# Performance work log

Hardware: AMD Instinct MI355X
Metric: run time of the kernel (lower is better)

The kernel has to match this reference:

```python
import jax, jax.numpy as jnp
import numpy as np

N = 10000
E = 160000
B = 16
NEG_SLOPE = 0.2


def gat_conv(x, src, dst, W, a_src, a_dst, b, heads, ch):
    # x: [N, F_in]; src/dst: [E'] (self-loops included); W: [F_in, heads*ch]
    n = x.shape[0]
    h = (x @ W).reshape(n, heads, ch)                     # [N,H,C]
    alpha_src = jnp.sum(h * a_src, axis=-1)               # [N,H]
    alpha_dst = jnp.sum(h * a_dst, axis=-1)               # [N,H]
    e = jax.nn.leaky_relu(alpha_src[src] + alpha_dst[dst], NEG_SLOPE)  # [E,H]
    # segment softmax over edges grouped by destination node
    m = jax.ops.segment_max(e, dst, num_segments=n)       # [N,H]
    ex = jnp.exp(e - m[dst])                              # [E,H]
    denom = jax.ops.segment_sum(ex, dst, num_segments=n)  # [N,H]
    alpha = ex / denom[dst]                               # [E,H]
    out = jax.ops.segment_sum(alpha[:, :, None] * h[src], dst, num_segments=n)  # [N,H,C]
    return out.reshape(n, heads * ch) + b


def setup_inputs() -> dict:
    key = jax.random.key(0)
    ks = jax.random.split(key, 16)
    glorot = lambda k, shp: jax.random.normal(k, shp, jnp.float32) * np.sqrt(2.0 / (shp[0] + shp[-1]))
    inp = {
        "x": jax.random.normal(ks[0], (N, 128), jnp.float32),
        "edge_index": jax.random.randint(ks[1], (2, E), 0, N, jnp.int64),
        "batch": jnp.sort(jax.random.randint(ks[2], (N,), 0, B, jnp.int64)),
        # conv1: 128 -> 128 per head, 8 heads
        "W1": glorot(ks[3], (128, 8 * 128)),
        "att_src1": glorot(ks[4], (8, 128)),
        "att_dst1": glorot(ks[5], (8, 128)),
        "b1": jnp.zeros((8 * 128,), jnp.float32),
        # conv2: 1024 -> 64 per head, 8 heads
        "W2": glorot(ks[6], (1024, 8 * 64)),
        "att_src2": glorot(ks[7], (8, 64)),
        "att_dst2": glorot(ks[8], (8, 64)),
        "b2": jnp.zeros((8 * 64,), jnp.float32),
        "fc1_w": glorot(ks[9], (512, 32)),
        "fc1_b": jnp.zeros((32,), jnp.float32),
        "fc2_w": glorot(ks[10], (32, 10)),
        "fc2_b": jnp.zeros((10,), jnp.float32),
    }
    return inp


def reference(x, edge_index, batch, W1, att_src1, att_dst1, b1,
              W2, att_src2, att_dst2, b2, fc1_w, fc1_b, fc2_w, fc2_b):
    n = x.shape[0]
    loop = jnp.arange(n, dtype=edge_index.dtype)
    src = jnp.concatenate([edge_index[0], loop])  # PyG add_self_loops=True
    dst = jnp.concatenate([edge_index[1], loop])
    h = jax.nn.elu(gat_conv(x, src, dst, W1, att_src1, att_dst1, b1, 8, 128))   # [N,1024]
    h = jax.nn.elu(gat_conv(h, src, dst, W2, att_src2, att_dst2, b2, 8, 64))    # [N,512]
    # global mean pool over graphs
    sums = jax.ops.segment_sum(h, batch, num_segments=B)                        # [B,512]
    cnt = jax.ops.segment_sum(jnp.ones((n,), h.dtype), batch, num_segments=B)
    g = sums / jnp.maximum(cnt, 1.0)[:, None]
    g = jax.nn.elu(g @ fc1_w + fc1_b)
    return g @ fc2_w + fc2_b                                                    # [B,10]
```

## Files before the change

### kernel.cpp

```cpp
#include <hip/hip_runtime.h>
#include <math.h>

#define HEADS 8
#define NEG 0.2f

typedef unsigned short ushort_t;
typedef __attribute__((ext_vector_type(8))) short short8;
typedef float f32x4 __attribute__((ext_vector_type(4)));

__device__ inline ushort_t f2bf(float f) {
  union { float f; unsigned u; } v; v.f = f;
  unsigned r = (v.u + 0x7FFF + ((v.u >> 16) & 1)) >> 16;
  return (ushort_t)r;
}

__device__ inline float4 bf4(uint2 v) {
  union { unsigned u; float f; } a, b, c, d;
  a.u = v.x << 16; b.u = v.x & 0xffff0000u;
  c.u = v.y << 16; d.u = v.y & 0xffff0000u;
  return make_float4(a.f, b.f, c.f, d.f);
}

__device__ inline float elu_f(float v) {
  return (v > 0.f) ? v : (__expf(v) - 1.f);
}

__global__ void zero_k(int* __restrict__ p, int n) {
  int i = blockIdx.x * blockDim.x + threadIdx.x;
  int stride = gridDim.x * blockDim.x;
  for (; i < n; i += stride) p[i] = 0;
}

__global__ void prep_k(const int* __restrict__ ei, int* __restrict__ src,
                       int* __restrict__ dst, int* __restrict__ deg, int E, int Nn) {
  int i = blockIdx.x * blockDim.x + threadIdx.x;
  if (i >= E + Nn) return;
  int s, d;
  if (i < E) { s = ei[i]; d = ei[E + i]; }
  else       { s = d = i - E; }
  src[i] = s;
  dst[i] = d;
  atomicAdd(&deg[d], 1);
}

__global__ __launch_bounds__(1024) void scan_k(const int* __restrict__ deg,
                                               int* __restrict__ offs,
                                               int* __restrict__ cursor, int Nn) {
  __shared__ int wtot[16];
  __shared__ int wexcl[16];
  __shared__ int soff_s;
  int t = threadIdx.x;
  int lane = t & 63, w = t >> 6;
  if (t == 0) soff_s = 0;
  __syncthreads();
  for (int base = 0; base < Nn; base += 4096) {
    int idx = base + 4 * t;
    int4 v = make_int4(0, 0, 0, 0);
    if (idx + 3 < Nn) v = *(const int4*)&deg[idx];
    else {
      if (idx < Nn)     v.x = deg[idx];
      if (idx + 1 < Nn) v.y = deg[idx + 1];
      if (idx + 2 < Nn) v.z = deg[idx + 2];
      if (idx + 3 < Nn) v.w = deg[idx + 3];
    }
    int s1 = v.x, s2 = s1 + v.y, s3 = s2 + v.z, s4 = s3 + v.w;
    int sc = s4;
#pragma unroll
    for (int o = 1; o < 64; o <<= 1) {
      int x = __shfl_up(sc, o);
      if (lane >= o) sc += x;
    }
    if (lane == 63) wtot[w] = sc;
    __syncthreads();
    if (w == 0) {
      int tv = (lane < 16) ? wtot[lane] : 0;
      int ts = tv;
#pragma unroll
      for (int o = 1; o < 16; o <<= 1) {
        int x = __shfl_up(ts, o);
        if (lane >= o) ts += x;
      }
      if (lane < 16) wexcl[lane] = ts - tv;
      if (lane == 15) wtot[15] = ts;
    }
    __syncthreads();
    int excl = soff_s + wexcl[w] + (sc - s4);
    int o0 = excl, o1 = excl + s1, o2 = excl + s2, o3 = excl + s3;
    if (idx < Nn)     { offs[idx] = o0;     cursor[idx] = o0; }
    if (idx + 1 < Nn) { offs[idx + 1] = o1; cursor[idx + 1] = o1; }
    if (idx + 2 < Nn) { offs[idx + 2] = o2; cursor[idx + 2] = o2; }
    if (idx + 3 < Nn) { offs[idx + 3] = o3; cursor[idx + 3] = o3; }
    int chunk_total = wtot[15];
    __syncthreads();
    if (t == 0) soff_s += chunk_total;
    __syncthreads();
  }
  if (t == 0) offs[Nn] = soff_s;
}

__global__ void scatter_k(const int* __restrict__ src, const int* __restrict__ dst,
                          int* __restrict__ cursor, int* __restrict__ psrc, int Etot) {
  int i = blockIdx.x * blockDim.x + threadIdx.x;
  if (i >= Etot) return;
  int p = atomicAdd(&cursor[dst[i]], 1);
  psrc[p] = src[i];
}

__global__ void cast_k(const float* __restrict__ in, ushort_t* __restrict__ out, int n4) {
  int i = blockIdx.x * blockDim.x + threadIdx.x;
  if (i >= n4) return;
  float4 v = ((const float4*)in)[i];
  ushort_t o[4] = {f2bf(v.x), f2bf(v.y), f2bf(v.z), f2bf(v.w)};
  *(uint2*)&out[i * 4] = *(uint2*)o;
}

__global__ void tcast_k(const float* __restrict__ W, ushort_t* __restrict__ Wt, int K, int N) {
  int idx = blockIdx.x * blockDim.x + threadIdx.x;
  if (idx >= K * N) return;
  int n = idx / K, k = idx - n * K;
  Wt[idx] = f2bf(W[(size_t)k * N + n]);
}

#define LDA 40
__global__ __launch_bounds__(256) void mfma_gemm_k(const ushort_t* __restrict__ A,
                                                   const ushort_t* __restrict__ Bt,
                                                   ushort_t* __restrict__ Cb,
                                                   const float* __restrict__ att_s,
                                                   const float* __restrict__ att_d,
                                                   float* __restrict__ asrc,
                                                   float* __restrict__ adst,
                                                   int M, int N, int K, int CSHIFT) {
  __shared__ ushort_t As[128 * LDA];
  __shared__ ushort_t Bs[128 * LDA];
  int tid = threadIdx.x;
  int lane = tid & 63;
  int wave = tid >> 6;
  int wm = (wave >> 1) * 64, wn = (wave & 1) * 64;
  int bm = blockIdx.y * 128, bn = blockIdx.x * 128;
  int lrow = lane & 15, lq = lane >> 4;

  f32x4 acc[4][4];
#pragma unroll
  for (int i = 0; i < 4; i++)
#pragma unroll
    for (int j = 0; j < 4; j++) acc[i][j] = 0.f;

  int srow = tid >> 2;
  int skc = (tid & 3) * 8;

  int gr0 = min(bm + srow, M - 1);
  int gr1 = min(bm + srow + 64, M - 1);
  const ushort_t* pa0 = &A[(size_t)gr0 * K + skc];
  const ushort_t* pa1 = &A[(size_t)gr1 * K + skc];
  const ushort_t* pb0 = &Bt[(size_t)(bn + srow) * K + skc];
  const ushort_t* pb1 = &Bt[(size_t)(bn + srow + 64) * K + skc];

  short8 va0 = *(const short8*)pa0;
  short8 va1 = *(const short8*)pa1;
  short8 vb0 = *(const short8*)pb0;
  short8 vb1 = *(const short8*)pb1;

  for (int k0 = 0; k0 < K; k0 += 32) {
    __syncthreads();
    *(short8*)&As[srow * LDA + skc] = va0;
    *(short8*)&As[(srow + 64) * LDA + skc] = va1;
    *(short8*)&Bs[srow * LDA + skc] = vb0;
    *(short8*)&Bs[(srow + 64) * LDA + skc] = vb1;
    __syncthreads();
    if (k0 + 32 < K) {
      va0 = *(const short8*)(pa0 + k0 + 32);
      va1 = *(const short8*)(pa1 + k0 + 32);
      vb0 = *(const short8*)(pb0 + k0 + 32);
      vb1 = *(const short8*)(pb1 + k0 + 32);
    }
    short8 af[4], bfr[4];
#pragma unroll
    for (int t = 0; t < 4; t++) {
      af[t]  = *(const short8*)&As[(wm + t * 16 + lrow) * LDA + lq * 8];
      bfr[t] = *(const short8*)&Bs[(wn + t * 16 + lrow) * LDA + lq * 8];
    }
#pragma unroll
    for (int i = 0; i < 4; i++)
#pragma unroll
      for (int j = 0; j < 4; j++)
        acc[i][j] = __builtin_amdgcn_mfma_f32_16x16x32_bf16(af[i], bfr[j], acc[i][j], 0, 0, 0);
  }

  {
    int hh = (bn + wn) >> CSHIFT;
    float avs[4], avd[4];
#pragma unroll
    for (int j = 0; j < 4; j++) {
      int col = bn + wn + j * 16 + lrow;
      avs[j] = att_s[col];
      avd[j] = att_d[col];
    }
#pragma unroll
    for (int i = 0; i < 4; i++) {
#pragma unroll
      for (int r = 0; r < 4; r++) {
        float ps = 0.f, pd = 0.f;
#pragma unroll
        for (int j = 0; j < 4; j++) {
          float v = acc[i][j][r];
          ps += v * avs[j];
          pd += v * avd[j];
        }
#pragma unroll
        for (int o = 1; o < 16; o <<= 1) {
          ps += __shfl_xor(ps, o);
          pd += __shfl_xor(pd, o);
        }
        int row = bm + wm + i * 16 + lq * 4 + r;
        if (lrow == 0 && row < M) {
          atomicAdd(&asrc[row * HEADS + hh], ps);
          atomicAdd(&adst[row * HEADS + hh], pd);
        }
      }
    }
  }

#pragma unroll
  for (int i = 0; i < 4; i++) {
    int row0 = bm + wm + i * 16 + lq * 4;
#pragma unroll
    for (int j = 0; j < 4; j++) {
      int col = bn + wn + j * 16 + lrow;
#pragma unroll
      for (int r = 0; r < 4; r++) {
        int row = row0 + r;
        if (row < M) Cb[(size_t)row * N + col] = f2bf(acc[i][j][r]);
      }
    }
  }
}

template <int F, int CSHIFT, int BT, int NSPLIT, typename OT>
__global__ __launch_bounds__(BT) void aggregate_k(const ushort_t* __restrict__ hb,
                                                  const float* __restrict__ asrc,
                                                  const float* __restrict__ adst,
                                                  const int* __restrict__ offs,
                                                  const int* __restrict__ psrc,
                                                  const float* __restrict__ bias,
                                                  OT* __restrict__ out) {
  constexpr int CPB = F / NSPLIT;
  static_assert(CPB == 4 * BT, "CPB/thread mismatch");
  int nb = blockIdx.x;
  int n = nb / NSPLIT;
  int coff = (nb - n * NSPLIT) * CPB;
  int t = threadIdx.x;
  int c0 = coff + 4 * t;
  int hh = c0 >> CSHIFT;
  float adn = adst[n * HEADS + hh];
  int e0 = offs[n], e1 = offs[n + 1];
  float4 acc = make_float4(0.f, 0.f, 0.f, 0.f);
  float wsum = 0.f;

  int i = e0;
  int s[8];
  if (i + 8 <= e1) {
#pragma unroll
    for (int u = 0; u < 8; u++) s[u] = psrc[i + u];
  }
  while (i + 8 <= e1) {
    uint2 r[8];
    float av[8];
#pragma unroll
    for (int u = 0; u < 8; u++) r[u] = *(const uint2*)&hb[(size_t)s[u] * F + c0];
#pragma unroll
    for (int u = 0; u < 8; u++) av[u] = asrc[s[u] * HEADS + hh];
    i += 8;
    bool more = (i + 8 <= e1);
    int sn[8];
#pragma unroll
    for (int u = 0; u < 8; u++) sn[u] = more ? psrc[i + u] : 0;
#pragma unroll
    for (int u = 0; u < 8; u++) {
      float v = av[u] + adn;
      v = (v > 0.f) ? v : NEG * v;
      float w = __expf(v);
      float4 f = bf4(r[u]);
      wsum += w;
      acc.x += w * f.x;
      acc.y += w * f.y;
      acc.z += w * f.z;
      acc.w += w * f.w;
    }
#pragma unroll
    for (int u = 0; u < 8; u++) s[u] = sn[u];
  }
  for (; i < e1; i++) {
    int ss = psrc[i];
    float v = asrc[ss * HEADS + hh] + adn;
    v = (v > 0.f) ? v : NEG * v;
    float w = __expf(v);
    float4 f = bf4(*(const uint2*)&hb[(size_t)ss * F + c0]);
    wsum += w;
    acc.x += w * f.x; acc.y += w * f.y;
    acc.z += w * f.z; acc.w += w * f.w;
  }

  float inv = 1.f / wsum;
  float v0 = elu_f(acc.x * inv + bias[c0]);
  float v1 = elu_f(acc.y * inv + bias[c0 + 1]);
  float v2 = elu_f(acc.z * inv + bias[c0 + 2]);
  float v3 = elu_f(acc.w * inv + bias[c0 + 3]);
  if (sizeof(OT) == 2) {
    unsigned p0 = (unsigned)f2bf(v0) | ((unsigned)f2bf(v1) << 16);
    unsigned p1 = (unsigned)f2bf(v2) | ((unsigned)f2bf(v3) << 16);
    *(uint2*)&((ushort_t*)out)[(size_t)n * F + c0] = make_uint2(p0, p1);
  } else {
    *(float4*)&((float*)out)[(size_t)n * F + c0] = make_float4(v0, v1, v2, v3);
  }
}

__global__ void bounds_k(const int* __restrict__ batch, int* __restrict__ bstart,
                         int* __restrict__ bend, int Nn) {
  int i = blockIdx.x * blockDim.x + threadIdx.x;
  if (i >= Nn) return;
  int b = batch[i];
  if (i == 0 || batch[i - 1] != b) bstart[b] = i;
  if (i == Nn - 1 || batch[i + 1] != b) bend[b] = i + 1;
}

__global__ __launch_bounds__(256) void pool_k(const float* __restrict__ g,
                                              const int* __restrict__ batch,
                                              float* __restrict__ sums, int Nn) {
  int c = blockIdx.x * 256 + threadIdx.x;
  int n0 = blockIdx.y * 50;
  int n1 = min(n0 + 50, Nn);
  if (n0 >= n1) return;
  float acc = 0.f;
  int cur = batch[n0];
  for (int n = n0; n < n1; n++) {
    int b = batch[n];
    if (b != cur) { atomicAdd(&sums[cur * 512 + c], acc); acc = 0.f; cur = b; }
    acc += g[(size_t)n * 512 + c];
  }
  atomicAdd(&sums[cur * 512 + c], acc);
}

__global__ __launch_bounds__(512) void mlp_k(const float* __restrict__ sums,
                                             const int* __restrict__ bstart,
                                             const int* __restrict__ bend,
                                             const float* __restrict__ w1,
                                             const float* __restrict__ b1,
                                             const float* __restrict__ w2,
                                             const float* __restrict__ b2,
                                             float* __restrict__ out) {
  __shared__ float gm[16 * 512];
  __shared__ float t1[16 * 32];
  int t = threadIdx.x;
  for (int i = t; i < 16 * 512; i += 512) {
    int b = i >> 9;
    float c = (float)(bend[b] - bstart[b]);
    gm[i] = sums[i] / fmaxf(c, 1.f);
  }
  __syncthreads();
  {
    int b = t >> 5, j = t & 31;
    float s = b1[j];
    for (int k = 0; k < 512; k++) s += gm[(b << 9) + k] * w1[k * 32 + j];
    t1[t] = elu_f(s);
  }
  __syncthreads();
  if (t < 160) {
    int b = t / 10, j = t - b * 10;
    float s = b2[j];
#pragma unroll
    for (int k = 0; k < 32; k++) s += t1[b * 32 + k] * w2[k * 10 + j];
    out[t] = s;
  }
}

extern "C" void kernel_launch(void* const* d_in, const int* in_sizes, int n_in,
                              void* d_out, int out_size, void* d_ws, size_t ws_size,
                              hipStream_t stream) {
  const float* x   = (const float*)d_in[0];
  const int*   ei  = (const int*)d_in[1];
  const int* batch = (const int*)d_in[2];
  const float* W1  = (const float*)d_in[3];
  const float* as1 = (const float*)d_in[4];
  const float* ad1 = (const float*)d_in[5];
  const float* b1  = (const float*)d_in[6];
  const float* W2  = (const float*)d_in[7];
  const float* as2 = (const float*)d_in[8];
  const float* ad2 = (const float*)d_in[9];
  const float* b2  = (const float*)d_in[10];
  const float* f1w = (const float*)d_in[11];
  const float* f1b = (const float*)d_in[12];
  const float* f2w = (const float*)d_in[13];
  const float* f2b = (const float*)d_in[14];
  float* out = (float*)d_out;

  const int Nn = in_sizes[2];
  const int E = in_sizes[1] / 2;
  const int Etot = E + Nn;

  size_t off = 0;
  auto alloc = [&](size_t elems) { size_t o = off; off += (elems + 63) & ~(size_t)63; return o; };
  int* wsi = (int*)d_ws;
  float* wsf = (float*)d_ws;

  size_t o_deg  = alloc(Nn);
  size_t o_pool = alloc(16 * 512);
  size_t o_bst  = alloc(64);
  size_t o_ben  = alloc(64);
  size_t o_as1  = alloc((size_t)Nn * 8);
  size_t o_ad1  = alloc((size_t)Nn * 8);
  size_t o_as2  = alloc((size_t)Nn * 8);
  size_t o_ad2  = alloc((size_t)Nn * 8);
  size_t zero_words = off;
  size_t o_offs = alloc(Nn + 1);
  size_t o_cur  = alloc(Nn);
  size_t o_src  = alloc(Etot);
  size_t o_dst  = alloc(Etot);
  size_t o_psrc = alloc(Etot);
  size_t o_xb   = alloc((size_t)Nn * 128 / 2);
  size_t o_w1t  = alloc(1024 * 128 / 2);
  size_t o_w2t  = alloc(512 * 1024 / 2);
  size_t o_h    = alloc((size_t)Nn * 1024 / 2);
  size_t o_g    = alloc((size_t)Nn * 1024);

  ushort_t* xb  = (ushort_t*)(wsi + o_xb);
  ushort_t* w1t = (ushort_t*)(wsi + o_w1t);
  ushort_t* w2t = (ushort_t*)(wsi + o_w2t);
  ushort_t* hb  = (ushort_t*)(wsi + o_h);
  ushort_t* g1b = (ushort_t*)(wsi + o_g);

  int eb = (Etot + 255) / 256;

  zero_k<<<512, 256, 0, stream>>>(wsi, (int)zero_words);
  prep_k<<<eb, 256, 0, stream>>>(ei, wsi + o_src, wsi + o_dst, wsi + o_deg, E, Nn);
  scan_k<<<1, 1024, 0, stream>>>(wsi + o_deg, wsi + o_offs, wsi + o_cur, Nn);
  scatter_k<<<eb, 256, 0, stream>>>(wsi + o_src, wsi + o_dst, wsi + o_cur,
                                    wsi + o_psrc, Etot);

  cast_k<<<(Nn * 128 / 4 + 255) / 256, 256, 0, stream>>>(x, xb, Nn * 128 / 4);
  tcast_k<<<(128 * 1024 + 255) / 256, 256, 0, stream>>>(W1, w1t, 128, 1024);
  tcast_k<<<(1024 * 512 + 255) / 256, 256, 0, stream>>>(W2, w2t, 1024, 512);

  mfma_gemm_k<<<dim3(1024 / 128, (Nn + 127) / 128), 256, 0, stream>>>(
      xb, w1t, hb, as1, ad1, wsf + o_as1, wsf + o_ad1, Nn, 1024, 128, 7);
  aggregate_k<1024, 7, 128, 2, ushort_t><<<Nn * 2, 128, 0, stream>>>(
      hb, wsf + o_as1, wsf + o_ad1, wsi + o_offs, wsi + o_psrc, b1, g1b);

  mfma_gemm_k<<<dim3(512 / 128, (Nn + 127) / 128), 256, 0, stream>>>(
      g1b, w2t, hb, as2, ad2, wsf + o_as2, wsf + o_ad2, Nn, 512, 1024, 6);
  aggregate_k<512, 6, 64, 2, float><<<Nn * 2, 64, 0, stream>>>(
      hb, wsf + o_as2, wsf + o_ad2, wsi + o_offs, wsi + o_psrc, b2, wsf + o_g);

  bounds_k<<<(Nn + 255) / 256, 256, 0, stream>>>(batch, wsi + o_bst, wsi + o_ben, Nn);
  pool_k<<<dim3(2, (Nn + 49) / 50), 256, 0, stream>>>(wsf + o_g, batch, wsf + o_pool, Nn);
  mlp_k<<<1, 512, 0, stream>>>(wsf + o_pool, wsi + o_bst, wsi + o_ben, f1w, f1b, f2w, f2b, out);
}
```

Baseline: 284.8 us.

## Fuse cast/bounds launches into existing kernels and double GEMM K-tile to 64

Result: faster. 277.8 us (-2.5%).

```diff
diff --git a/kernel.cpp b/kernel.cpp
--- a/kernel.cpp
+++ b/kernel.cpp
@@ -32,8 +32,15 @@
 }
 
 __global__ void prep_k(const int* __restrict__ ei, int* __restrict__ src,
-                       int* __restrict__ dst, int* __restrict__ deg, int E, int Nn) {
+                       int* __restrict__ dst, int* __restrict__ deg,
+                       const int* __restrict__ batch, int* __restrict__ bstart,
+                       int* __restrict__ bend, int E, int Nn) {
   int i = blockIdx.x * blockDim.x + threadIdx.x;
+  if (i < Nn) {
+    int b = batch[i];
+    if (i == 0 || batch[i - 1] != b) bstart[b] = i;
+    if (i == Nn - 1 || batch[i + 1] != b) bend[b] = i + 1;
+  }
   if (i >= E + Nn) return;
   int s, d;
   if (i < E) { s = ei[i]; d = ei[E + i]; }
@@ -106,22 +113,27 @@
   psrc[p] = src[i];
 }
 
-__global__ void cast_k(const float* __restrict__ in, ushort_t* __restrict__ out, int n4) {
+__global__ void castall_k(const float* __restrict__ x, ushort_t* __restrict__ xb,
+                          const float* __restrict__ W1, ushort_t* __restrict__ w1t,
+                          const float* __restrict__ W2, ushort_t* __restrict__ w2t,
+                          int nx4) {
   int i = blockIdx.x * blockDim.x + threadIdx.x;
-  if (i >= n4) return;
-  float4 v = ((const float4*)in)[i];
-  ushort_t o[4] = {f2bf(v.x), f2bf(v.y), f2bf(v.z), f2bf(v.w)};
-  *(uint2*)&out[i * 4] = *(uint2*)o;
-}
-
-__global__ void tcast_k(const float* __restrict__ W, ushort_t* __restrict__ Wt, int K, int N) {
-  int idx = blockIdx.x * blockDim.x + threadIdx.x;
-  if (idx >= K * N) return;
-  int n = idx / K, k = idx - n * K;
-  Wt[idx] = f2bf(W[(size_t)k * N + n]);
-}
-
-#define LDA 40
+  if (i < nx4) {
+    float4 v = ((const float4*)x)[i];
+    ushort_t o[4] = {f2bf(v.x), f2bf(v.y), f2bf(v.z), f2bf(v.w)};
+    *(uint2*)&xb[i * 4] = *(uint2*)o;
+  }
+  if (i < 128 * 1024) {
+    int n = i >> 7, k = i & 127;
+    w1t[i] = f2bf(W1[(size_t)k * 1024 + n]);
+  }
+  if (i < 1024 * 512) {
+    int n = i >> 10, k = i & 1023;
+    w2t[i] = f2bf(W2[(size_t)k * 512 + n]);
+  }
+}
+
+#define LDA 72
 __global__ __launch_bounds__(256) void mfma_gemm_k(const ushort_t* __restrict__ A,
                                                    const ushort_t* __restrict__ Bt,
                                                    ushort_t* __restrict__ Cb,
@@ -156,34 +168,50 @@
   const ushort_t* pb1 = &Bt[(size_t)(bn + srow + 64) * K + skc];
 
   short8 va0 = *(const short8*)pa0;
-  short8 va1 = *(const short8*)pa1;
+  short8 va1 = *(const short8*)(pa0 + 32);
+  short8 va2 = *(const short8*)pa1;
+  short8 va3 = *(const short8*)(pa1 + 32);
   short8 vb0 = *(const short8*)pb0;
-  short8 vb1 = *(const short8*)pb1;
-
-  for (int k0 = 0; k0 < K; k0 += 32) {
+  short8 vb1 = *(const short8*)(pb0 + 32);
+  short8 vb2 = *(const short8*)pb1;
+  short8 vb3 = *(const short8*)(pb1 + 32);
+
+  for (int k0 = 0; k0 < K; k0 += 64) {
     __syncthreads();
     *(short8*)&As[srow * LDA + skc] = va0;
-    *(short8*)&As[(srow + 64) * LDA + skc] = va1;
+    *(short8*)&As[srow * LDA + 32 + skc] = va1;
+    *(short8*)&As[(srow + 64) * LDA + skc] = va2;
+    *(short8*)&As[(srow + 64) * LDA + 32 + skc] = va3;
     *(short8*)&Bs[srow * LDA + skc] = vb0;
-    *(short8*)&Bs[(srow + 64) * LDA + skc] = vb1;
-    __syncthreads();
-    if (k0 + 32 < K) {
-      va0 = *(const short8*)(pa0 + k0 + 32);
-      va1 = *(const short8*)(pa1 + k0 + 32);
-      vb0 = *(const short8*)(pb0 + k0 + 32);
-      vb1 = *(const short8*)(pb1 + k0 + 32);
-    }
-    short8 af[4], bfr[4];
-#pragma unroll
-    for (int t = 0; t < 4; t++) {
-      af[t]  = *(const short8*)&As[(wm + t * 16 + lrow) * LDA + lq * 8];
-      bfr[t] = *(const short8*)&Bs[(wn + t * 16 + lrow) * LDA + lq * 8];
-    }
-#pragma unroll
-    for (int i = 0; i < 4; i++)
-#pragma unroll
-      for (int j = 0; j < 4; j++)
-        acc[i][j] = __builtin_amdgcn_mfma_f32_16x16x32_bf16(af[i], bfr[j], acc[i][j], 0, 0, 0);
+    *(short8*)&Bs[srow * LDA + 32 + skc] = vb1;
+    *(short8*)&Bs[(srow + 64) * LDA + skc] = vb2;
+    *(short8*)&Bs[(srow + 64) * LDA + 32 + skc] = vb3;
+    __syncthreads();
+    if (k0 + 64 < K) {
+      int kn = k0 + 64;
+      va0 = *(const short8*)(pa0 + kn);
+      va1 = *(const short8*)(pa0 + kn + 32);
+      va2 = *(const short8*)(pa1 + kn);
+      va3 = *(const short8*)(pa1 + kn + 32);
+      vb0 = *(const short8*)(pb0 + kn);
+      vb1 = *(const short8*)(pb0 + kn + 32);
+      vb2 = *(const short8*)(pb1 + kn);
+      vb3 = *(const short8*)(pb1 + kn + 32);
+    }
+#pragma unroll
+    for (int ks = 0; ks < 2; ks++) {
+      short8 af[4], bfr[4];
+#pragma unroll
+      for (int t = 0; t < 4; t++) {
+        af[t]  = *(const short8*)&As[(wm + t * 16 + lrow) * LDA + ks * 32 + lq * 8];
+        bfr[t] = *(const short8*)&Bs[(wn + t * 16 + lrow) * LDA + ks * 32 + lq * 8];
+      }
+#pragma unroll
+      for (int i = 0; i < 4; i++)
+#pragma unroll
+        for (int j = 0; j < 4; j++)
+          acc[i][j] = __builtin_amdgcn_mfma_f32_16x16x32_bf16(af[i], bfr[j], acc[i][j], 0, 0, 0);
+    }
   }
 
   {
@@ -314,15 +342,6 @@
   }
 }
 
-__global__ void bounds_k(const int* __restrict__ batch, int* __restrict__ bstart,
-                         int* __restrict__ bend, int Nn) {
-  int i = blockIdx.x * blockDim.x + threadIdx.x;
-  if (i >= Nn) return;
-  int b = batch[i];
-  if (i == 0 || batch[i - 1] != b) bstart[b] = i;
-  if (i == Nn - 1 || batch[i + 1] != b) bend[b] = i + 1;
-}
-
 __global__ __launch_bounds__(256) void pool_k(const float* __restrict__ g,
                                               const int* __restrict__ batch,
                                               float* __restrict__ sums, int Nn) {
@@ -404,13 +423,13 @@
 
   size_t o_deg  = alloc(Nn);
   size_t o_pool = alloc(16 * 512);
-  size_t o_bst  = alloc(64);
-  size_t o_ben  = alloc(64);
   size_t o_as1  = alloc((size_t)Nn * 8);
   size_t o_ad1  = alloc((size_t)Nn * 8);
   size_t o_as2  = alloc((size_t)Nn * 8);
   size_t o_ad2  = alloc((size_t)Nn * 8);
   size_t zero_words = off;
+  size_t o_bst  = alloc(64);
+  size_t o_ben  = alloc(64);
   size_t o_offs = alloc(Nn + 1);
   size_t o_cur  = alloc(Nn);
   size_t o_src  = alloc(Etot);
@@ -431,14 +450,14 @@
   int eb = (Etot + 255) / 256;
 
   zero_k<<<512, 256, 0, stream>>>(wsi, (int)zero_words);
-  prep_k<<<eb, 256, 0, stream>>>(ei, wsi + o_src, wsi + o_dst, wsi + o_deg, E, Nn);
+  prep_k<<<eb, 256, 0, stream>>>(ei, wsi + o_src, wsi + o_dst, wsi + o_deg,
+                                 batch, wsi + o_bst, wsi + o_ben, E, Nn);
   scan_k<<<1, 1024, 0, stream>>>(wsi + o_deg, wsi + o_offs, wsi + o_cur, Nn);
   scatter_k<<<eb, 256, 0, stream>>>(wsi + o_src, wsi + o_dst, wsi + o_cur,
                                     wsi + o_psrc, Etot);
 
-  cast_k<<<(Nn * 128 / 4 + 255) / 256, 256, 0, stream>>>(x, xb, Nn * 128 / 4);
-  tcast_k<<<(128 * 1024 + 255) / 256, 256, 0, stream>>>(W1, w1t, 128, 1024);
-  tcast_k<<<(1024 * 512 + 255) / 256, 256, 0, stream>>>(W2, w2t, 1024, 512);
+  castall_k<<<(1024 * 512 + 255) / 256, 256, 0, stream>>>(x, xb, W1, w1t, W2, w2t,
+                                                          Nn * 128 / 4);
 
   mfma_gemm_k<<<dim3(1024 / 128, (Nn + 127) / 128), 256, 0, stream>>>(
       xb, w1t, hb, as1, ad1, wsf + o_as1, wsf + o_ad1, Nn, 1024, 128, 7);
@@ -450,7 +469,6 @@
   aggregate_k<512, 6, 64, 2, float><<<Nn * 2, 64, 0, stream>>>(
       hb, wsf + o_as2, wsf + o_ad2, wsi + o_offs, wsi + o_psrc, b2, wsf + o_g);
 
-  bounds_k<<<(Nn + 255) / 256, 256, 0, stream>>>(batch, wsi + o_bst, wsi + o_ben, Nn);
   pool_k<<<dim3(2, (Nn + 49) / 50), 256, 0, stream>>>(wsf + o_g, batch, wsf + o_pool, Nn);
   mlp_k<<<1, 512, 0, stream>>>(wsf + o_pool, wsi + o_bst, wsi + o_ben, f1w, f1b, f2w, f2b, out);
 }
```
